# Kernel optimization log

Hardware: AMD Instinct MI355X
Metric: run time of the kernel (lower is better)

## Reference

```python
import jax, jax.numpy as jnp
import numpy as np

B = 32
HIST, C, H, W = 10, 11, 15, 20
D, NH, NL = 256, 4, 4
HD = D // NH
OUT, ADIM = 256, 20
L = HIST * H * W + 1  # 3001 tokens incl. cls
VIS = HIST * C * H * W  # 33000


def layernorm(x, g, b, eps=1e-5):
    m = jnp.mean(x, axis=-1, keepdims=True)
    v = jnp.mean((x - m) ** 2, axis=-1, keepdims=True)
    return (x - m) * jax.lax.rsqrt(v + eps) * g + b


def rope_1d(x):
    # x: [B, NH, L, HD]
    l, hd = x.shape[2], x.shape[3]
    t = jnp.arange(l, dtype=x.dtype)
    freqs = 10000.0 ** (-jnp.arange(0, hd, 2, dtype=x.dtype) / hd)
    emb = t[:, None] * freqs[None, :]            # [L, HD/2]
    emb = jnp.concatenate([emb, emb], axis=-1)   # [L, HD]
    cos = jnp.cos(emb)[None, None]
    sin = jnp.sin(emb)[None, None]
    x1, x2 = x[..., : hd // 2], x[..., hd // 2 :]
    rot = jnp.concatenate([-x2, x1], axis=-1)
    return x * cos + rot * sin


def lightning_attn(x, qw, kw, vw, ow, gq, bq, gk, bk):
    b, l, _ = x.shape
    q = layernorm(x @ qw, gq, bq)
    k = layernorm(x @ kw, gk, bk)
    v = x @ vw
    split = lambda a: a.reshape(b, l, NH, HD).transpose(0, 2, 1, 3)  # [B,NH,L,HD]
    q, k, v = split(q), split(k), split(v)
    q = jax.nn.silu(rope_1d(q))
    k = jax.nn.silu(rope_1d(k))
    kv = jnp.einsum('bhld,bhle->bhde', k, v)            # O(L) kv accumulation
    out = jnp.einsum('bhld,bhde->bhle', q, kv)
    out = out / jnp.sqrt(jnp.asarray(HD, x.dtype))
    out = out.transpose(0, 2, 1, 3).reshape(b, l, D)
    return out @ ow


def forward(obs_stack, proj_w, proj_b, cls_token, qw, kw, vw, ow, gq, bq, gk, bk,
            n1g, n1b, n2g, n2b, w1, b1, w2, b2, fng, fnb, out_w, out_b):
    b = obs_stack.shape[0]
    obs_feat = obs_stack[:, :VIS]
    action_feat = obs_stack[:, VIS:]
    vision = obs_feat.reshape(b, HIST, C, H, W).transpose(0, 1, 3, 4, 2)  # [B,T,H,W,C]
    x = vision @ proj_w + proj_b                                          # [B,T,H,W,D]
    x = x.reshape(b, -1, D)
    cls = jnp.broadcast_to(cls_token, (b, 1, D))
    x = jnp.concatenate([cls, x], axis=1)                                 # [B,L,D]
    for i in range(NL):
        h = lightning_attn(layernorm(x, n1g[i], n1b[i]), qw[i], kw[i], vw[i], ow[i],
                           gq[i], bq[i], gk[i], bk[i])
        x = x + h
        y = layernorm(x, n2g[i], n2b[i])
        y = jax.nn.gelu(y @ w1[i] + b1[i], approximate=False) @ w2[i] + b2[i]
        x = x + y
    x = layernorm(x, fng, fnb)
    cls_out = x[:, 0, :]
    final = jnp.concatenate([cls_out, action_feat], axis=1)
    return final @ out_w + out_b


def setup_inputs() -> dict:
    key = jax.random.key(0)
    ks = jax.random.split(key, 16)
    s = 0.02
    n = lambda k, shp: jax.random.normal(k, shp, dtype=jnp.float32) * s
    inp = {
        'obs_stack': jax.random.normal(ks[0], (B, VIS + ADIM), dtype=jnp.float32),
        'proj_w': n(ks[1], (C, D)),
        'proj_b': jnp.zeros((D,), jnp.float32),
        'cls_token': jax.random.normal(ks[2], (1, 1, D), dtype=jnp.float32),
        'qw': n(ks[3], (NL, D, D)),
        'kw': n(ks[4], (NL, D, D)),
        'vw': n(ks[5], (NL, D, D)),
        'ow': n(ks[6], (NL, D, D)),
        'gq': jnp.ones((NL, D), jnp.float32),
        'bq': jnp.zeros((NL, D), jnp.float32),
        'gk': jnp.ones((NL, D), jnp.float32),
        'bk': jnp.zeros((NL, D), jnp.float32),
        'n1g': jnp.ones((NL, D), jnp.float32),
        'n1b': jnp.zeros((NL, D), jnp.float32),
        'n2g': jnp.ones((NL, D), jnp.float32),
        'n2b': jnp.zeros((NL, D), jnp.float32),
        'w1': n(ks[7], (NL, D, 4 * D)),
        'b1': jnp.zeros((NL, 4 * D), jnp.float32),
        'w2': n(ks[8], (NL, 4 * D, D)),
        'b2': jnp.zeros((NL, D), jnp.float32),
        'fng': jnp.ones((D,), jnp.float32),
        'fnb': jnp.zeros((D,), jnp.float32),
        'out_w': n(ks[9], (D + ADIM, OUT)),
        'out_b': jnp.zeros((OUT,), jnp.float32),
    }
    return inp


def reference(obs_stack, proj_w, proj_b, cls_token, qw, kw, vw, ow, gq, bq, gk, bk,
              n1g, n1b, n2g, n2b, w1, b1, w2, b2, fng, fnb, out_w, out_b):
    return forward(obs_stack, proj_w, proj_b, cls_token, qw, kw, vw, ow, gq, bq, gk, bk,
                   n1g, n1b, n2g, n2b, w1, b1, w2, b2, fng, fnb, out_w, out_b)
```

## Files before the change

### kernel.cpp

```cpp
#include <hip/hip_runtime.h>
#include <math.h>

typedef unsigned short u16;
typedef __attribute__((ext_vector_type(8))) short short8;
typedef __attribute__((ext_vector_type(4))) short short4v;
typedef __attribute__((ext_vector_type(4))) float f32x4;

constexpr int B_    = 32;
constexpr int HIST_ = 10, C_ = 11, H_ = 15, W_ = 20;
constexpr int D_    = 256, NH_ = 4, NL_ = 4, HD_ = 64;
constexpr int OUT_  = 256, ADIM_ = 20;
constexpr int L_    = HIST_*H_*W_ + 1;
constexpr int VIS_  = HIST_*C_*H_*W_;
constexpr int NTOK  = B_*L_;
constexpr int OBSROW = VIS_ + ADIM_;
constexpr int PADR  = 128;

__device__ __forceinline__ float bf2f(u16 u) {
    return __uint_as_float(((unsigned)u) << 16);
}
__device__ __forceinline__ u16 f2bf(float f) {
    unsigned u = __float_as_uint(f);
    u = u + 0x7FFFu + ((u >> 16) & 1u);
    return (u16)(u >> 16);
}
__device__ __forceinline__ f32x4 mfma16(short8 a, short8 b, f32x4 c) {
    return __builtin_amdgcn_mfma_f32_16x16x32_bf16(a, b, c, 0, 0, 0);
}
__device__ __forceinline__ void gload16(const u16* gsrc, u16* ldsdst) {
    __builtin_amdgcn_global_load_lds(
        (const __attribute__((address_space(1))) unsigned int*)gsrc,
        (__attribute__((address_space(3))) unsigned int*)ldsdst,
        16, 0, 0);
}
__device__ __forceinline__ float gelu_fast(float v) {
    float t2 = 1.5957691216f*(v + 0.044715f*v*v*v);
    return v / (1.f + __expf(-t2));
}

__global__ void zero_kernel(float* __restrict__ p, int n) {
    int i = blockIdx.x*256 + threadIdx.x;
    if (i < n) p[i] = 0.f;
}

__global__ void wcvt_kernel(const float* __restrict__ src, u16* __restrict__ dst,
                            int Nn, int Kk, int dstLS, int dstOff) {
    int idx = blockIdx.x*256 + threadIdx.x;
    int tot = NL_*Nn*Kk;
    if (idx >= tot) return;
    int l = idx / (Nn*Kk);
    int rem = idx % (Nn*Kk);
    int n = rem / Kk, k = rem % Kk;
    dst[(size_t)l*dstLS + (size_t)(dstOff+n)*Kk + k] = f2bf(src[(size_t)l*Kk*Nn + (size_t)k*Nn + n]);
}

__global__ void rope_table_kernel(float* __restrict__ tab) {
    int idx = blockIdx.x*256 + threadIdx.x;
    if (idx >= L_*32) return;
    int t = idx >> 5, i = idx & 31;
    float freq = powf(10000.f, -2.f*(float)i/(float)HD_);
    float ang = (float)t * freq;
    tab[idx*2]   = cosf(ang);
    tab[idx*2+1] = sinf(ang);
}

__global__ __launch_bounds__(256) void proj_kernel(const float* __restrict__ obs,
        const float* __restrict__ pw, const float* __restrict__ pb,
        const float* __restrict__ cls, float* __restrict__ x) {
    int wave = threadIdx.x >> 6, lane = threadIdx.x & 63;
    int n = blockIdx.x*4 + wave;
    if (n >= NTOK) return;
    int b = n / L_, l = n % L_;
    float4 acc;
    if (l == 0) {
        acc = ((const float4*)cls)[lane];
    } else {
        int t = l - 1;
        int hist = t / (H_*W_);
        int rem  = t % (H_*W_);
        float vv = 0.f;
        if (lane < C_) vv = obs[(size_t)b*OBSROW + hist*(C_*H_*W_) + lane*(H_*W_) + rem];
        acc = ((const float4*)pb)[lane];
        #pragma unroll
        for (int c = 0; c < C_; ++c) {
            float vc = __shfl(vv, c);
            float4 w4 = ((const float4*)(pw + c*D_))[lane];
            acc.x += vc*w4.x; acc.y += vc*w4.y; acc.z += vc*w4.z; acc.w += vc*w4.w;
        }
    }
    ((float4*)(x + (size_t)n*D_))[lane] = acc;
}

__global__ __launch_bounds__(256) void ln_f2b_kernel(const float* __restrict__ in,
        const float* __restrict__ g, const float* __restrict__ bt,
        u16* __restrict__ out, int ntok) {
    int wave = threadIdx.x >> 6, lane = threadIdx.x & 63;
    int n = blockIdx.x*4 + wave;
    if (n >= ntok) return;
    float4 v = ((const float4*)(in + (size_t)n*D_))[lane];
    float s  = v.x + v.y + v.z + v.w;
    float sq = v.x*v.x + v.y*v.y + v.z*v.z + v.w*v.w;
    #pragma unroll
    for (int off = 32; off; off >>= 1) { s += __shfl_xor(s, off); sq += __shfl_xor(sq, off); }
    float mean = s * (1.f/D_);
    float var  = sq * (1.f/D_) - mean*mean;
    float r = rsqrtf(var + 1e-5f);
    float4 gg = ((const float4*)g)[lane];
    float4 bb = ((const float4*)bt)[lane];
    short4v o;
    o.x = (short)f2bf((v.x-mean)*r*gg.x + bb.x);
    o.y = (short)f2bf((v.y-mean)*r*gg.y + bb.y);
    o.z = (short)f2bf((v.z-mean)*r*gg.z + bb.z);
    o.w = (short)f2bf((v.w-mean)*r*gg.w + bb.w);
    *(short4v*)(out + (size_t)n*D_ + lane*4) = o;
}

__global__ __launch_bounds__(256) void lnres_kernel(float* __restrict__ x,
        u16* __restrict__ dx, const float* __restrict__ g, const float* __restrict__ bt,
        int ntok) {
    int wave = threadIdx.x >> 6, lane = threadIdx.x & 63;
    int n = blockIdx.x*4 + wave;
    if (n >= ntok) return;
    float4 v = ((const float4*)(x + (size_t)n*D_))[lane];
    short4v d = *(const short4v*)(dx + (size_t)n*D_ + lane*4);
    v.x += bf2f((u16)d.x); v.y += bf2f((u16)d.y);
    v.z += bf2f((u16)d.z); v.w += bf2f((u16)d.w);
    ((float4*)(x + (size_t)n*D_))[lane] = v;
    float s  = v.x + v.y + v.z + v.w;
    float sq = v.x*v.x + v.y*v.y + v.z*v.z + v.w*v.w;
    #pragma unroll
    for (int off = 32; off; off >>= 1) { s += __shfl_xor(s, off); sq += __shfl_xor(sq, off); }
    float mean = s * (1.f/D_);
    float var  = sq * (1.f/D_) - mean*mean;
    float r = rsqrtf(var + 1e-5f);
    float4 gg = ((const float4*)g)[lane];
    float4 bb = ((const float4*)bt)[lane];
    short4v o;
    o.x = (short)f2bf((v.x-mean)*r*gg.x + bb.x);
    o.y = (short)f2bf((v.y-mean)*r*gg.y + bb.y);
    o.z = (short)f2bf((v.z-mean)*r*gg.z + bb.z);
    o.w = (short)f2bf((v.w-mean)*r*gg.w + bb.w);
    *(short4v*)(dx + (size_t)n*D_ + lane*4) = o;
}

__global__ __launch_bounds__(256) void lnrope_kernel(u16* __restrict__ qk,
        const float* __restrict__ gq, const float* __restrict__ bq,
        const float* __restrict__ gk, const float* __restrict__ bk,
        const float* __restrict__ tab, int ntok, int ld) {
    u16* q = qk + blockIdx.y*256;
    const float* g  = blockIdx.y ? gk : gq;
    const float* bt = blockIdx.y ? bk : bq;
    int wave = threadIdx.x >> 6, lane = threadIdx.x & 63;
    int n = blockIdx.x*4 + wave;
    if (n >= ntok) return;
    int l = n % L_;
    short4v raw = *(const short4v*)(q + (size_t)n*ld + lane*4);
    float v0 = bf2f((u16)raw.x), v1 = bf2f((u16)raw.y), v2 = bf2f((u16)raw.z), v3 = bf2f((u16)raw.w);
    float s  = v0+v1+v2+v3;
    float sq = v0*v0+v1*v1+v2*v2+v3*v3;
    #pragma unroll
    for (int off = 32; off; off >>= 1) { s += __shfl_xor(s, off); sq += __shfl_xor(sq, off); }
    float mean = s * (1.f/D_);
    float var  = sq * (1.f/D_) - mean*mean;
    float r = rsqrtf(var + 1e-5f);
    float4 gg = ((const float4*)g)[lane];
    float4 bb = ((const float4*)bt)[lane];
    float o0 = (v0-mean)*r*gg.x + bb.x;
    float o1 = (v1-mean)*r*gg.y + bb.y;
    float o2 = (v2-mean)*r*gg.z + bb.z;
    float o3 = (v3-mean)*r*gg.w + bb.w;
    float p0 = __shfl_xor(o0, 8), p1 = __shfl_xor(o1, 8);
    float p2 = __shfl_xor(o2, 8), p3 = __shfl_xor(o3, 8);
    bool first = (lane & 15) < 8;
    const float4* tp = (const float4*)(tab + ((size_t)l*32 + (lane&7)*4)*2);
    float4 t01 = tp[0], t23 = tp[1];
    float r0 = first ? o0*t01.x - p0*t01.y : o0*t01.x + p0*t01.y;
    float r1 = first ? o1*t01.z - p1*t01.w : o1*t01.z + p1*t01.w;
    float r2 = first ? o2*t23.x - p2*t23.y : o2*t23.x + p2*t23.y;
    float r3 = first ? o3*t23.z - p3*t23.w : o3*t23.z + p3*t23.w;
    r0 = r0 / (1.f + expf(-r0));
    r1 = r1 / (1.f + expf(-r1));
    r2 = r2 / (1.f + expf(-r2));
    r3 = r3 / (1.f + expf(-r3));
    short4v o;
    o.x = (short)f2bf(r0); o.y = (short)f2bf(r1);
    o.z = (short)f2bf(r2); o.w = (short)f2bf(r3);
    *(short4v*)(q + (size_t)n*ld + lane*4) = o;
}

template<int EPI, bool PB>
__global__ __launch_bounds__(256) void gemm_bf16(const u16* __restrict__ A, int lda,
        const u16* __restrict__ Wt, const float* __restrict__ bias,
        u16* __restrict__ Cb, float* __restrict__ Xres, int M, int N, int K, int ldc) {
    __shared__ u16 As[2*128*32];
    __shared__ u16 Bs[2*128*32];
    const int gx = gridDim.x;
    int n = blockIdx.y * gx + blockIdx.x;
    const int nwg = gx * gridDim.y;
    if ((nwg & 7) == 0) n = (n & 7) * (nwg >> 3) + (n >> 3);
    const int bx = n % gx, by = n / gx;
    const int row0 = by*128, col0 = bx*128;

    size_t zrow = 0;
    if (PB) {
        int z = blockIdx.z;
        A  += (size_t)z * M * lda;
        Wt += (size_t)z * N * K;
        zrow = (size_t)z * M;
    }

    const int tid = threadIdx.x;
    const int wid = tid >> 6, lane = tid & 63;
    const int wr = wid >> 1, wc = wid & 1;

    f32x4 acc[4][4];
    #pragma unroll
    for (int i = 0; i < 4; ++i)
        #pragma unroll
        for (int j = 0; j < 4; ++j) {
            f32x4 z; z.x = 0.f; z.y = 0.f; z.z = 0.f; z.w = 0.f;
            acc[i][j] = z;
        }

    const int r0s = wid*32 + (lane>>2);
    const int r1s = r0s + 16;
    const int s0 = ((lane&3) - (r0s>>1)) & 3;
    const int s1 = ((lane&3) - (r1s>>1)) & 3;
    const u16* a0p = A  + (size_t)(row0 + r0s)*lda + s0*8;
    const u16* a1p = A  + (size_t)(row0 + r1s)*lda + s1*8;
    const u16* b0p = Wt + (size_t)(col0 + r0s)*K + s0*8;
    const u16* b1p = Wt + (size_t)(col0 + r1s)*K + s1*8;
    u16* lA0 = As + (wid*2+0)*512;
    u16* lA1 = As + (wid*2+1)*512;
    u16* lB0 = Bs + (wid*2+0)*512;
    u16* lB1 = Bs + (wid*2+1)*512;

    const int kg = lane >> 4, li = lane & 15;
    int aoff[4], boff[4];
    #pragma unroll
    for (int mi = 0; mi < 4; ++mi) {
        int row = wr*64 + mi*16 + li;
        aoff[mi] = row*32 + ((kg + (row>>1)) & 3)*8;
    }
    #pragma unroll
    for (int ni = 0; ni < 4; ++ni) {
        int row = wc*64 + ni*16 + li;
        boff[ni] = row*32 + ((kg + (row>>1)) & 3)*8;
    }

    auto stage = [&](int k0) {
        #pragma unroll
        for (int t = 0; t < 2; ++t) {
            const int ko = k0 + t*32;
            const int lo = t*4096;
            gload16(a0p + ko, lA0 + lo); gload16(a1p + ko, lA1 + lo);
            gload16(b0p + ko, lB0 + lo); gload16(b1p + ko, lB1 + lo);
        }
    };

    stage(0);
    const int nk2 = K >> 6;
    for (int ks = 0; ks < nk2; ++ks) {
        __syncthreads();
        short8 af[2][4], bfr[2][4];
        #pragma unroll
        for (int t = 0; t < 2; ++t) {
            #pragma unroll
            for (int mi = 0; mi < 4; ++mi) af[t][mi] = *(const short8*)(As + t*4096 + aoff[mi]);
            #pragma unroll
            for (int ni = 0; ni < 4; ++ni) bfr[t][ni] = *(const short8*)(Bs + t*4096 + boff[ni]);
        }
        __syncthreads();
        if (ks + 1 < nk2) stage((ks + 1) << 6);
        #pragma unroll
        for (int t = 0; t < 2; ++t)
            #pragma unroll
            for (int mi = 0; mi < 4; ++mi)
                #pragma unroll
                for (int ni = 0; ni < 4; ++ni)
                    acc[mi][ni] = mfma16(af[t][mi], bfr[t][ni], acc[mi][ni]);
    }

    #pragma unroll
    for (int mi = 0; mi < 4; ++mi) {
        int rbase = row0 + wr*64 + mi*16 + kg*4;
        #pragma unroll
        for (int ni = 0; ni < 4; ++ni) {
            int col = col0 + wc*64 + ni*16 + li;
            #pragma unroll
            for (int r = 0; r < 4; ++r) {
                int row = rbase + r;
                if (row >= M) continue;
                float v = acc[mi][ni][r];
                if (EPI == 1 || EPI == 4) v += bias[col];
                if (EPI == 1) v = gelu_fast(v);
                Cb[(zrow + row)*(size_t)ldc + col] = f2bf(v);
            }
        }
    }
}

template<int EPI, bool PB>
__global__ __launch_bounds__(512) void gemm_wide(const u16* __restrict__ A, int lda,
        const u16* __restrict__ Wt, const float* __restrict__ bias,
        u16* __restrict__ Cb, int M, int N, int K, int ldc) {
    __shared__ u16 As[2*4096];
    __shared__ u16 Bs[2*8192];
    const int gx = gridDim.x;
    int n = blockIdx.y * gx + blockIdx.x;
    const int nwg = gx * gridDim.y;
    if ((nwg & 7) == 0) n = (n & 7) * (nwg >> 3) + (n >> 3);
    const int bx = n % gx, by = n / gx;
    const int row0 = by*128, col0 = bx*256;

    size_t zrow = 0;
    if (PB) {
        int z = blockIdx.z;
        A  += (size_t)z * M * lda;
        Wt += (size_t)z * N * K;
        zrow = (size_t)z * M;
    }

    const int tid = threadIdx.x;
    const int wid = tid >> 6, lane = tid & 63;
    const int kg = lane >> 4, li = lane & 15;

    f32x4 acc[16];
    #pragma unroll
    for (int i = 0; i < 16; ++i) { f32x4 z; z.x=0.f; z.y=0.f; z.z=0.f; z.w=0.f; acc[i]=z; }

    const int ra = wid*16 + (lane>>2);
    const int sa = ((lane&3) - (ra>>1)) & 3;
    const u16* agp = A + (size_t)(row0 + ra)*lda + sa*8;
    const int lAo = wid*512;
    const int rb0 = (wid*2+0)*16 + (lane>>2);
    const int rb1 = (wid*2+1)*16 + (lane>>2);
    const int sb0 = ((lane&3) - (rb0>>1)) & 3;
    const int sb1 = ((lane&3) - (rb1>>1)) & 3;
    const u16* bgp0 = Wt + (size_t)(col0 + rb0)*K + sb0*8;
    const u16* bgp1 = Wt + (size_t)(col0 + rb1)*K + sb1*8;
    const int lB0o = (wid*2+0)*512;
    const int lB1o = (wid*2+1)*512;

    const int arow = wid*16 + li;
    const int aoff = arow*32 + ((kg + (arow>>1)) & 3)*8;
    int boff[16];
    #pragma unroll
    for (int ni = 0; ni < 16; ++ni) {
        int row = ni*16 + li;
        boff[ni] = row*32 + ((kg + (row>>1)) & 3)*8;
    }

    auto stage = [&](int k0) {
        #pragma unroll
        for (int t = 0; t < 2; ++t) {
            const int ko = k0 + t*32;
            gload16(agp  + ko, As + t*4096 + lAo);
            gload16(bgp0 + ko, Bs + t*8192 + lB0o);
            gload16(bgp1 + ko, Bs + t*8192 + lB1o);
        }
    };

    stage(0);
    const int nk2 = K >> 6;
    for (int ks = 0; ks < nk2; ++ks) {
        __syncthreads();
        short8 af0 = *(const short8*)(As + aoff);
        short8 b0[8], b1[8];
        #pragma unroll
        for (int ni = 0; ni < 8; ++ni) b0[ni] = *(const short8*)(Bs + boff[ni]);
        #pragma unroll
        for (int ni = 0; ni < 8; ++ni) acc[ni] = mfma16(af0, b0[ni], acc[ni]);
        #pragma unroll
        for (int ni = 0; ni < 8; ++ni) b1[ni] = *(const short8*)(Bs + boff[8+ni]);
        #pragma unroll
        for (int ni = 0; ni < 8; ++ni) acc[8+ni] = mfma16(af0, b1[ni], acc[8+ni]);
        short8 af1 = *(const short8*)(As + 4096 + aoff);
        #pragma unroll
        for (int ni = 0; ni < 8; ++ni) b0[ni] = *(const short8*)(Bs + 8192 + boff[ni]);
        #pragma unroll
        for (int ni = 0; ni < 8; ++ni) b1[ni] = *(const short8*)(Bs + 8192 + boff[8+ni]);
        __syncthreads();
        if (ks + 1 < nk2) stage((ks + 1) << 6);
        #pragma unroll
        for (int ni = 0; ni < 8; ++ni) acc[ni]   = mfma16(af1, b0[ni], acc[ni]);
        #pragma unroll
        for (int ni = 0; ni < 8; ++ni) acc[8+ni] = mfma16(af1, b1[ni], acc[8+ni]);
    }

    #pragma unroll
    for (int r = 0; r < 4; ++r) {
        const int row = row0 + wid*16 + kg*4 + r;
        if (row >= M) continue;
        #pragma unroll
        for (int ni = 0; ni < 16; ++ni) {
            int col = col0 + ni*16 + li;
            float v = acc[ni][r];
            if (EPI == 1) { v += bias[col]; v = gelu_fast(v); }
            Cb[(zrow + row)*(size_t)ldc + col] = f2bf(v);
        }
    }
}

constexpr int KV_LSPLIT = 4;
constexpr int KV_PART   = 768;
__global__ __launch_bounds__(256) void kv_mfma_kernel(const u16* __restrict__ Kt,
        const u16* __restrict__ Vt, float* __restrict__ kvf, int ld) {
    __shared__ u16 kT[64][34];
    __shared__ u16 vT[64][34];
    const int bh = blockIdx.x;
    const int b = bh >> 2, h = bh & 3;
    const int tid = threadIdx.x;
    const int wid = tid >> 6, lane = tid & 63;
    const int kg = lane >> 4, li = lane & 15;
    const int wm = (wid >> 1)*32, wn = (wid & 1)*32;
    const int sl = tid >> 3;
    const int sd = (tid & 7) * 8;
    const u16* kbase = Kt + ((size_t)b*L_)*ld + h*HD_ + sd;
    const u16* vbase = Vt + ((size_t)b*L_)*ld + h*HD_ + sd;

    f32x4 acc[2][2];
    #pragma unroll
    for (int i = 0; i < 2; ++i)
        #pragma unroll
        for (int j = 0; j < 2; ++j) {
            f32x4 z; z.x=0.f; z.y=0.f; z.z=0.f; z.w=0.f; acc[i][j] = z;
        }

    const int l0p = blockIdx.y * KV_PART;
    for (int t = 0; t < KV_PART/32; ++t) {
        int gl = l0p + t*32 + sl;
        short8 kk = {0,0,0,0,0,0,0,0}, vv = {0,0,0,0,0,0,0,0};
        if (gl < L_) {
            kk = *(const short8*)(kbase + (size_t)gl*ld);
            vv = *(const short8*)(vbase + (size_t)gl*ld);
        }
        __syncthreads();
        #pragma unroll
        for (int j = 0; j < 8; ++j) {
            kT[sd+j][sl] = (u16)kk[j];
            vT[sd+j][sl] = (u16)vv[j];
        }
        __syncthreads();
        short8 a0, a1, b0, b1;
        {
            uint* d0 = (uint*)&a0; const uint* p0 = (const uint*)&kT[wm + li][kg*8];
            uint* d1 = (uint*)&a1; const uint* p1 = (const uint*)&kT[wm + 16 + li][kg*8];
            uint* d2 = (uint*)&b0; const uint* p2 = (const uint*)&vT[wn + li][kg*8];
            uint* d3 = (uint*)&b1; const uint* p3 = (const uint*)&vT[wn + 16 + li][kg*8];
            #pragma unroll
            for (int j = 0; j < 4; ++j) { d0[j]=p0[j]; d1[j]=p1[j]; d2[j]=p2[j]; d3[j]=p3[j]; }
        }
        acc[0][0] = mfma16(a0, b0, acc[0][0]);
        acc[0][1] = mfma16(a0, b1, acc[0][1]);
        acc[1][0] = mfma16(a1, b0, acc[1][0]);
        acc[1][1] = mfma16(a1, b1, acc[1][1]);
    }
    float* base = kvf + (size_t)bh*4096;
    #pragma unroll
    for (int mi = 0; mi < 2; ++mi)
        #pragma unroll
        for (int ni = 0; ni < 2; ++ni)
            #pragma unroll
            for (int r = 0; r < 4; ++r)
                atomicAdd(base + (wm + mi*16 + kg*4 + r)*64 + wn + ni*16 + li,
                          acc[mi][ni][r]);
}

__global__ __launch_bounds__(256) void m2_kernel(const float* __restrict__ kvf,
        const float* __restrict__ ow, u16* __restrict__ m2t) {
    __shared__ float kvs[64][64];
    const int bh = blockIdx.x;
    const int b = bh >> 2, h = bh & 3;
    const int tid = threadIdx.x;
    #pragma unroll
    for (int p = 0; p < 16; ++p)
        ((float*)kvs)[p*256 + tid] = kvf[(size_t)bh*4096 + p*256 + tid];
    __syncthreads();
    float acc[64];
    #pragma unroll
    for (int d = 0; d < 64; ++d) acc[d] = 0.f;
    for (int e = 0; e < 64; ++e) {
        float w = ow[(size_t)(h*64 + e)*256 + tid];
        #pragma unroll
        for (int d = 0; d < 64; ++d) acc[d] += kvs[d][e] * w;
    }
    u16* dst = m2t + ((size_t)b*256 + tid)*256 + h*64;
    #pragma unroll
    for (int d = 0; d < 64; ++d) dst[d] = f2bf(acc[d]*0.125f);
}

__global__ __launch_bounds__(256) void tail_kernel(const u16* __restrict__ Xn,
        const u16* __restrict__ qwT,
        const float* __restrict__ gqv, const float* __restrict__ bqv,
        const u16* __restrict__ m2t, float* __restrict__ x,
        const float* __restrict__ g2, const float* __restrict__ bt2,
        const u16* __restrict__ w1T, const float* __restrict__ b1v,
        const u16* __restrict__ w2T, const float* __restrict__ b2v) {
    __shared__ float xn0[256];
    __shared__ float qrow[256];
    __shared__ float y[256];
    __shared__ float h[1024];
    __shared__ float red[8];
    const int bl = blockIdx.x;
    const int tid = threadIdx.x;
    const int wave = tid >> 6, lane = tid & 63;
    const size_t row = (size_t)bl * L_;
    xn0[tid] = bf2f(Xn[row*256 + tid]);
    __syncthreads();
    {
        const u16* qwrow = qwT + (size_t)tid*256;
        float qa = 0.f;
        for (int k = 0; k < 256; k += 8) {
            short8 w = *(const short8*)(qwrow + k);
            qa += xn0[k+0]*bf2f((u16)w[0]) + xn0[k+1]*bf2f((u16)w[1])
                + xn0[k+2]*bf2f((u16)w[2]) + xn0[k+3]*bf2f((u16)w[3])
                + xn0[k+4]*bf2f((u16)w[4]) + xn0[k+5]*bf2f((u16)w[5])
                + xn0[k+6]*bf2f((u16)w[6]) + xn0[k+7]*bf2f((u16)w[7]);
        }
        float s = qa, sq = qa*qa;
        #pragma unroll
        for (int off = 32; off; off >>= 1) { s += __shfl_xor(s, off); sq += __shfl_xor(sq, off); }
        if (lane == 0) { red[wave] = s; red[4+wave] = sq; }
        __syncthreads();
        s  = red[0]+red[1]+red[2]+red[3];
        sq = red[4]+red[5]+red[6]+red[7];
        float mean = s*(1.f/256.f), var = sq*(1.f/256.f) - mean*mean;
        float rstd = rsqrtf(var + 1e-5f);
        float qn = (qa - mean)*rstd*gqv[tid] + bqv[tid];
        qrow[tid] = qn / (1.f + __expf(-qn));
    }
    __syncthreads();
    const u16* mrow = m2t + ((size_t)bl*256 + tid)*256;
    float acc = 0.f;
    for (int d = 0; d < 256; d += 8) {
        short8 w = *(const short8*)(mrow + d);
        acc += qrow[d+0]*bf2f((u16)w[0]) + qrow[d+1]*bf2f((u16)w[1])
             + qrow[d+2]*bf2f((u16)w[2]) + qrow[d+3]*bf2f((u16)w[3])
             + qrow[d+4]*bf2f((u16)w[4]) + qrow[d+5]*bf2f((u16)w[5])
             + qrow[d+6]*bf2f((u16)w[6]) + qrow[d+7]*bf2f((u16)w[7]);
    }
    float v = x[row*256 + tid] + acc;
    float s = v, sq = v*v;
    #pragma unroll
    for (int off = 32; off; off >>= 1) { s += __shfl_xor(s, off); sq += __shfl_xor(sq, off); }
    if (lane == 0) { red[wave] = s; red[4+wave] = sq; }
    __syncthreads();
    s  = red[0]+red[1]+red[2]+red[3];
    sq = red[4]+red[5]+red[6]+red[7];
    float mean = s*(1.f/256.f), var = sq*(1.f/256.f) - mean*mean;
    float rstd = rsqrtf(var + 1e-5f);
    y[tid] = (v - mean)*rstd*g2[tid] + bt2[tid];
    __syncthreads();
    #pragma unroll
    for (int jj = 0; jj < 4; ++jj) {
        int j = tid*4 + jj;
        const u16* wrow = w1T + (size_t)j*256;
        float a = b1v[j];
        for (int k = 0; k < 256; k += 8) {
            short8 w = *(const short8*)(wrow + k);
            a += y[k+0]*bf2f((u16)w[0]) + y[k+1]*bf2f((u16)w[1])
               + y[k+2]*bf2f((u16)w[2]) + y[k+3]*bf2f((u16)w[3])
               + y[k+4]*bf2f((u16)w[4]) + y[k+5]*bf2f((u16)w[5])
               + y[k+6]*bf2f((u16)w[6]) + y[k+7]*bf2f((u16)w[7]);
        }
        h[j] = gelu_fast(a);
    }
    __syncthreads();
    const u16* w2row = w2T + (size_t)tid*1024;
    float a2 = b2v[tid];
    for (int k = 0; k < 1024; k += 8) {
        short8 w = *(const short8*)(w2row + k);
        a2 += h[k+0]*bf2f((u16)w[0]) + h[k+1]*bf2f((u16)w[1])
            + h[k+2]*bf2f((u16)w[2]) + h[k+3]*bf2f((u16)w[3])
            + h[k+4]*bf2f((u16)w[4]) + h[k+5]*bf2f((u16)w[5])
            + h[k+6]*bf2f((u16)w[6]) + h[k+7]*bf2f((u16)w[7]);
    }
    x[row*256 + tid] = v + a2;
}

__global__ void head_kernel(const float* __restrict__ x, const float* __restrict__ obs,
                            const float* __restrict__ fng, const float* __restrict__ fnb,
                            const float* __restrict__ ow, const float* __restrict__ ob,
                            float* __restrict__ out) {
    __shared__ float row[D_ + ADIM_];
    __shared__ float red[8];
    int b = blockIdx.x, tid = threadIdx.x;
    float v = x[((size_t)b*L_)*D_ + tid];
    float s = v, sq = v*v;
    #pragma unroll
    for (int off = 32; off; off >>= 1) { s += __shfl_xor(s, off); sq += __shfl_xor(sq, off); }
    int wave = tid >> 6, lane = tid & 63;
    if (lane == 0) { red[wave] = s; red[4+wave] = sq; }
    __syncthreads();
    s  = red[0]+red[1]+red[2]+red[3];
    sq = red[4]+red[5]+red[6]+red[7];
    float mean = s*(1.f/D_), var = sq*(1.f/D_) - mean*mean;
    float r = rsqrtf(var + 1e-5f);
    row[tid] = (v-mean)*r*fng[tid] + fnb[tid];
    if (tid < ADIM_) row[D_+tid] = obs[(size_t)b*OBSROW + VIS_ + tid];
    __syncthreads();
    float acc = ob[tid];
    for (int j = 0; j < D_+ADIM_; ++j) acc += row[j]*ow[j*OUT_ + tid];
    out[(size_t)b*OUT_ + tid] = acc;
}

extern "C" void kernel_launch(void* const* d_in, const int* in_sizes, int n_in,
                              void* d_out, int out_size, void* d_ws, size_t ws_size,
                              hipStream_t stream) {
    const float* obs   = (const float*)d_in[0];
    const float* pw    = (const float*)d_in[1];
    const float* pb    = (const float*)d_in[2];
    const float* cls   = (const float*)d_in[3];
    const float* qw    = (const float*)d_in[4];
    const float* kw    = (const float*)d_in[5];
    const float* vw    = (const float*)d_in[6];
    const float* oww   = (const float*)d_in[7];
    const float* gq    = (const float*)d_in[8];
    const float* bq    = (const float*)d_in[9];
    const float* gk    = (const float*)d_in[10];
    const float* bk    = (const float*)d_in[11];
    const float* n1g   = (const float*)d_in[12];
    const float* n1b   = (const float*)d_in[13];
    const float* n2g   = (const float*)d_in[14];
    const float* n2b   = (const float*)d_in[15];
    const float* w1    = (const float*)d_in[16];
    const float* b1    = (const float*)d_in[17];
    const float* w2    = (const float*)d_in[18];
    const float* b2    = (const float*)d_in[19];
    const float* fng   = (const float*)d_in[20];
    const float* fnb   = (const float*)d_in[21];
    const float* outw  = (const float*)d_in[22];
    const float* outb  = (const float*)d_in[23];

    float* x = (float*)d_ws;
    u16* qkvT = (u16*)(x + (size_t)NTOK*D_);
    u16* w1T  = qkvT + (size_t)NL_*768*256;
    u16* w2T  = w1T  + (size_t)NL_*262144;
    float* tab = (float*)(w2T + (size_t)NL_*262144);
    u16* bufs = (u16*)(tab + (size_t)L_*32*2);

    size_t fixedB = (size_t)((char*)bufs - (char*)d_ws);
    auto needed = [&](int nb) -> size_t {
        size_t t = (size_t)nb * L_;
        return fixedB + (t*256 + (size_t)PADR*256)*2 + (t*1024 + (size_t)PADR*1024)*2
               + (size_t)nb*65536*2 + (size_t)nb*NH_*4096*4;
    };
    int nbc = 32;
    while (nbc > 1 && needed(nbc) > ws_size) nbc >>= 1;
    const int nch = B_ / nbc;
    const int RCn = nbc * L_;

    u16* Xn   = bufs;
    u16* QKVc = Xn + (size_t)RCn*256 + (size_t)PADR*256;
    u16* Hc   = QKVc;
    u16* M2T  = QKVc + (size_t)RCn*1024 + (size_t)PADR*1024;
    float* kvf = (float*)(M2T + (size_t)nbc*65536);

    wcvt_kernel<<<(NL_*65536 + 255)/256, 256, 0, stream>>>(qw,  qkvT, 256, 256, 768*256, 0);
    wcvt_kernel<<<(NL_*65536 + 255)/256, 256, 0, stream>>>(kw,  qkvT, 256, 256, 768*256, 256);
    wcvt_kernel<<<(NL_*65536 + 255)/256, 256, 0, stream>>>(vw,  qkvT, 256, 256, 768*256, 512);
    wcvt_kernel<<<(NL_*262144 + 255)/256, 256, 0, stream>>>(w1, w1T, 1024, 256, 262144, 0);
    wcvt_kernel<<<(NL_*262144 + 255)/256, 256, 0, stream>>>(w2, w2T, 256, 1024, 262144, 0);
    rope_table_kernel<<<(L_*32 + 255)/256, 256, 0, stream>>>(tab);
    proj_kernel<<<(NTOK + 3)/4, 256, 0, stream>>>(obs, pw, pb, cls, x);

    const int gy  = (RCn + 127)/128;
    const int lnb = (RCn + 3)/4;
    const int nbh = nbc*NH_;

    for (int c = 0; c < nch; ++c) {
        float* xc = x + (size_t)c*RCn*D_;
        ln_f2b_kernel<<<lnb, 256, 0, stream>>>(xc, n1g, n1b, Xn, RCn);

        for (int layer = 0; layer < NL_; ++layer) {
            const u16* qkvT_l = qkvT + (size_t)layer*768*256;
            const u16* w1T_l  = w1T  + (size_t)layer*262144;
            const u16* w2T_l  = w2T  + (size_t)layer*262144;
            const float* ow_l = oww + (size_t)layer*65536;
            const float* b1_l = b1 + (size_t)layer*1024;
            const float* b2_l = b2 + (size_t)layer*D_;

            if (layer < NL_-1) {
                gemm_wide<0,false><<<dim3(3, gy), 512, 0, stream>>>(Xn, 256, qkvT_l, nullptr, QKVc, RCn, 768, 256, 768);
                lnrope_kernel<<<dim3(lnb, 2), 256, 0, stream>>>(QKVc, gq + layer*D_, bq + layer*D_,
                                                                gk + layer*D_, bk + layer*D_, tab, RCn, 768);
            } else {
                gemm_wide<0,false><<<dim3(2, gy), 512, 0, stream>>>(Xn, 256, qkvT_l + 65536, nullptr, QKVc + 256, RCn, 512, 256, 768);
                lnrope_kernel<<<dim3(lnb, 1), 256, 0, stream>>>(QKVc + 256, gk + layer*D_, bk + layer*D_,
                                                                gk + layer*D_, bk + layer*D_, tab, RCn, 768);
            }
            zero_kernel<<<(nbh*4096 + 255)/256, 256, 0, stream>>>(kvf, nbh*4096);
            kv_mfma_kernel<<<dim3(nbh, KV_LSPLIT), 256, 0, stream>>>(QKVc + 256, QKVc + 512, kvf, 768);
            m2_kernel<<<nbh, 256, 0, stream>>>(kvf, ow_l, M2T);

            if (layer < NL_-1) {
                gemm_bf16<0,true><<<dim3(2, 24, nbc), 256, 0, stream>>>(QKVc, 768, M2T, nullptr, Xn, nullptr, L_, 256, 256, 256);
                lnres_kernel<<<lnb, 256, 0, stream>>>(xc, Xn, n2g + layer*D_, n2b + layer*D_, RCn);
                gemm_wide<1,false><<<dim3(4, gy), 512, 0, stream>>>(Xn, 256, w1T_l, b1_l, Hc, RCn, 1024, 256, 1024);
                gemm_bf16<4,false><<<dim3(2, gy), 256, 0, stream>>>(Hc, 1024, w2T_l, b2_l, Xn, nullptr, RCn, 256, 1024, 256);
                lnres_kernel<<<lnb, 256, 0, stream>>>(xc, Xn, n1g + (layer+1)*D_, n1b + (layer+1)*D_, RCn);
            } else {
                tail_kernel<<<nbc, 256, 0, stream>>>(Xn, qkvT_l, gq + layer*D_, bq + layer*D_,
                                                     M2T, xc, n2g + layer*D_, n2b + layer*D_,
                                                     w1T_l, b1_l, w2T_l, b2_l);
            }
        }
    }

    head_kernel<<<B_, 256, 0, stream>>>(x, obs, fng, fnb, outw, outb, (float*)d_out);
}
```

Before: 2.245 ms.

## Store residual stream in bf16 and hoist kv accumulator zeroing

```diff
diff --git a/kernel.cpp b/kernel.cpp
--- a/kernel.cpp
+++ b/kernel.cpp
@@ -66,7 +66,7 @@
 
 __global__ __launch_bounds__(256) void proj_kernel(const float* __restrict__ obs,
         const float* __restrict__ pw, const float* __restrict__ pb,
-        const float* __restrict__ cls, float* __restrict__ x) {
+        const float* __restrict__ cls, u16* __restrict__ x) {
     int wave = threadIdx.x >> 6, lane = threadIdx.x & 63;
     int n = blockIdx.x*4 + wave;
     if (n >= NTOK) return;
@@ -88,18 +88,22 @@
             acc.x += vc*w4.x; acc.y += vc*w4.y; acc.z += vc*w4.z; acc.w += vc*w4.w;
         }
     }
-    ((float4*)(x + (size_t)n*D_))[lane] = acc;
-}
-
-__global__ __launch_bounds__(256) void ln_f2b_kernel(const float* __restrict__ in,
+    short4v o;
+    o.x = (short)f2bf(acc.x); o.y = (short)f2bf(acc.y);
+    o.z = (short)f2bf(acc.z); o.w = (short)f2bf(acc.w);
+    *(short4v*)(x + (size_t)n*D_ + lane*4) = o;
+}
+
+__global__ __launch_bounds__(256) void ln_f2b_kernel(const u16* __restrict__ in,
         const float* __restrict__ g, const float* __restrict__ bt,
         u16* __restrict__ out, int ntok) {
     int wave = threadIdx.x >> 6, lane = threadIdx.x & 63;
     int n = blockIdx.x*4 + wave;
     if (n >= ntok) return;
-    float4 v = ((const float4*)(in + (size_t)n*D_))[lane];
-    float s  = v.x + v.y + v.z + v.w;
-    float sq = v.x*v.x + v.y*v.y + v.z*v.z + v.w*v.w;
+    short4v raw = *(const short4v*)(in + (size_t)n*D_ + lane*4);
+    float v0 = bf2f((u16)raw.x), v1 = bf2f((u16)raw.y), v2 = bf2f((u16)raw.z), v3 = bf2f((u16)raw.w);
+    float s  = v0+v1+v2+v3;
+    float sq = v0*v0+v1*v1+v2*v2+v3*v3;
     #pragma unroll
     for (int off = 32; off; off >>= 1) { s += __shfl_xor(s, off); sq += __shfl_xor(sq, off); }
     float mean = s * (1.f/D_);
@@ -108,26 +112,31 @@
     float4 gg = ((const float4*)g)[lane];
     float4 bb = ((const float4*)bt)[lane];
     short4v o;
-    o.x = (short)f2bf((v.x-mean)*r*gg.x + bb.x);
-    o.y = (short)f2bf((v.y-mean)*r*gg.y + bb.y);
-    o.z = (short)f2bf((v.z-mean)*r*gg.z + bb.z);
-    o.w = (short)f2bf((v.w-mean)*r*gg.w + bb.w);
+    o.x = (short)f2bf((v0-mean)*r*gg.x + bb.x);
+    o.y = (short)f2bf((v1-mean)*r*gg.y + bb.y);
+    o.z = (short)f2bf((v2-mean)*r*gg.z + bb.z);
+    o.w = (short)f2bf((v3-mean)*r*gg.w + bb.w);
     *(short4v*)(out + (size_t)n*D_ + lane*4) = o;
 }
 
-__global__ __launch_bounds__(256) void lnres_kernel(float* __restrict__ x,
+__global__ __launch_bounds__(256) void lnres_kernel(u16* __restrict__ x,
         u16* __restrict__ dx, const float* __restrict__ g, const float* __restrict__ bt,
         int ntok) {
     int wave = threadIdx.x >> 6, lane = threadIdx.x & 63;
     int n = blockIdx.x*4 + wave;
     if (n >= ntok) return;
-    float4 v = ((const float4*)(x + (size_t)n*D_))[lane];
-    short4v d = *(const short4v*)(dx + (size_t)n*D_ + lane*4);
-    v.x += bf2f((u16)d.x); v.y += bf2f((u16)d.y);
-    v.z += bf2f((u16)d.z); v.w += bf2f((u16)d.w);
-    ((float4*)(x + (size_t)n*D_))[lane] = v;
-    float s  = v.x + v.y + v.z + v.w;
-    float sq = v.x*v.x + v.y*v.y + v.z*v.z + v.w*v.w;
+    short4v xv = *(const short4v*)(x + (size_t)n*D_ + lane*4);
+    short4v d  = *(const short4v*)(dx + (size_t)n*D_ + lane*4);
+    float v0 = bf2f((u16)xv.x) + bf2f((u16)d.x);
+    float v1 = bf2f((u16)xv.y) + bf2f((u16)d.y);
+    float v2 = bf2f((u16)xv.z) + bf2f((u16)d.z);
+    float v3 = bf2f((u16)xv.w) + bf2f((u16)d.w);
+    short4v xo;
+    xo.x = (short)f2bf(v0); xo.y = (short)f2bf(v1);
+    xo.z = (short)f2bf(v2); xo.w = (short)f2bf(v3);
+    *(short4v*)(x + (size_t)n*D_ + lane*4) = xo;
+    float s  = v0+v1+v2+v3;
+    float sq = v0*v0+v1*v1+v2*v2+v3*v3;
     #pragma unroll
     for (int off = 32; off; off >>= 1) { s += __shfl_xor(s, off); sq += __shfl_xor(sq, off); }
     float mean = s * (1.f/D_);
@@ -136,10 +145,10 @@
     float4 gg = ((const float4*)g)[lane];
     float4 bb = ((const float4*)bt)[lane];
     short4v o;
-    o.x = (short)f2bf((v.x-mean)*r*gg.x + bb.x);
-    o.y = (short)f2bf((v.y-mean)*r*gg.y + bb.y);
-    o.z = (short)f2bf((v.z-mean)*r*gg.z + bb.z);
-    o.w = (short)f2bf((v.w-mean)*r*gg.w + bb.w);
+    o.x = (short)f2bf((v0-mean)*r*gg.x + bb.x);
+    o.y = (short)f2bf((v1-mean)*r*gg.y + bb.y);
+    o.z = (short)f2bf((v2-mean)*r*gg.z + bb.z);
+    o.w = (short)f2bf((v3-mean)*r*gg.w + bb.w);
     *(short4v*)(dx + (size_t)n*D_ + lane*4) = o;
 }
 
@@ -493,7 +502,7 @@
 __global__ __launch_bounds__(256) void tail_kernel(const u16* __restrict__ Xn,
         const u16* __restrict__ qwT,
         const float* __restrict__ gqv, const float* __restrict__ bqv,
-        const u16* __restrict__ m2t, float* __restrict__ x,
+        const u16* __restrict__ m2t, u16* __restrict__ x,
         const float* __restrict__ g2, const float* __restrict__ bt2,
         const u16* __restrict__ w1T, const float* __restrict__ b1v,
         const u16* __restrict__ w2T, const float* __restrict__ b2v) {
@@ -540,7 +549,7 @@
              + qrow[d+4]*bf2f((u16)w[4]) + qrow[d+5]*bf2f((u16)w[5])
              + qrow[d+6]*bf2f((u16)w[6]) + qrow[d+7]*bf2f((u16)w[7]);
     }
-    float v = x[row*256 + tid] + acc;
+    float v = bf2f(x[row*256 + tid]) + acc;
     float s = v, sq = v*v;
     #pragma unroll
     for (int off = 32; off; off >>= 1) { s += __shfl_xor(s, off); sq += __shfl_xor(sq, off); }
@@ -576,17 +585,17 @@
             + h[k+4]*bf2f((u16)w[4]) + h[k+5]*bf2f((u16)w[5])
             + h[k+6]*bf2f((u16)w[6]) + h[k+7]*bf2f((u16)w[7]);
     }
-    x[row*256 + tid] = v + a2;
-}
-
-__global__ void head_kernel(const float* __restrict__ x, const float* __restrict__ obs,
+    x[row*256 + tid] = f2bf(v + a2);
+}
+
+__global__ void head_kernel(const u16* __restrict__ x, const float* __restrict__ obs,
                             const float* __restrict__ fng, const float* __restrict__ fnb,
                             const float* __restrict__ ow, const float* __restrict__ ob,
                             float* __restrict__ out) {
     __shared__ float row[D_ + ADIM_];
     __shared__ float red[8];
     int b = blockIdx.x, tid = threadIdx.x;
-    float v = x[((size_t)b*L_)*D_ + tid];
+    float v = bf2f(x[((size_t)b*L_)*D_ + tid]);
     float s = v, sq = v*v;
     #pragma unroll
     for (int off = 32; off; off >>= 1) { s += __shfl_xor(s, off); sq += __shfl_xor(sq, off); }
@@ -633,18 +642,19 @@
     const float* outw  = (const float*)d_in[22];
     const float* outb  = (const float*)d_in[23];
 
-    float* x = (float*)d_ws;
-    u16* qkvT = (u16*)(x + (size_t)NTOK*D_);
+    u16* x    = (u16*)d_ws;
+    u16* qkvT = x + (size_t)NTOK*D_;
     u16* w1T  = qkvT + (size_t)NL_*768*256;
     u16* w2T  = w1T  + (size_t)NL_*262144;
     float* tab = (float*)(w2T + (size_t)NL_*262144);
-    u16* bufs = (u16*)(tab + (size_t)L_*32*2);
+    float* kvf_all = tab + (size_t)L_*32*2;
+    u16* bufs = (u16*)(kvf_all + (size_t)NL_*B_*NH_*4096);
 
     size_t fixedB = (size_t)((char*)bufs - (char*)d_ws);
     auto needed = [&](int nb) -> size_t {
         size_t t = (size_t)nb * L_;
         return fixedB + (t*256 + (size_t)PADR*256)*2 + (t*1024 + (size_t)PADR*1024)*2
-               + (size_t)nb*65536*2 + (size_t)nb*NH_*4096*4;
+               + (size_t)nb*65536*2;
     };
     int nbc = 32;
     while (nbc > 1 && needed(nbc) > ws_size) nbc >>= 1;
@@ -655,7 +665,6 @@
     u16* QKVc = Xn + (size_t)RCn*256 + (size_t)PADR*256;
     u16* Hc   = QKVc;
     u16* M2T  = QKVc + (size_t)RCn*1024 + (size_t)PADR*1024;
-    float* kvf = (float*)(M2T + (size_t)nbc*65536);
 
     wcvt_kernel<<<(NL_*65536 + 255)/256, 256, 0, stream>>>(qw,  qkvT, 256, 256, 768*256, 0);
     wcvt_kernel<<<(NL_*65536 + 255)/256, 256, 0, stream>>>(kw,  qkvT, 256, 256, 768*256, 256);
@@ -663,6 +672,7 @@
     wcvt_kernel<<<(NL_*262144 + 255)/256, 256, 0, stream>>>(w1, w1T, 1024, 256, 262144, 0);
     wcvt_kernel<<<(NL_*262144 + 255)/256, 256, 0, stream>>>(w2, w2T, 256, 1024, 262144, 0);
     rope_table_kernel<<<(L_*32 + 255)/256, 256, 0, stream>>>(tab);
+    zero_kernel<<<(NL_*B_*NH_*4096 + 255)/256, 256, 0, stream>>>(kvf_all, NL_*B_*NH_*4096);
     proj_kernel<<<(NTOK + 3)/4, 256, 0, stream>>>(obs, pw, pb, cls, x);
 
     const int gy  = (RCn + 127)/128;
@@ -670,7 +680,7 @@
     const int nbh = nbc*NH_;
 
     for (int c = 0; c < nch; ++c) {
-        float* xc = x + (size_t)c*RCn*D_;
+        u16* xc = x + (size_t)c*RCn*D_;
         ln_f2b_kernel<<<lnb, 256, 0, stream>>>(xc, n1g, n1b, Xn, RCn);
 
         for (int layer = 0; layer < NL_; ++layer) {
@@ -680,6 +690,7 @@
             const float* ow_l = oww + (size_t)layer*65536;
             const float* b1_l = b1 + (size_t)layer*1024;
             const float* b2_l = b2 + (size_t)layer*D_;
+            float* kvf = kvf_all + ((size_t)(c*NL_ + layer))*nbh*4096;
 
             if (layer < NL_-1) {
                 gemm_wide<0,false><<<dim3(3, gy), 512, 0, stream>>>(Xn, 256, qkvT_l, nullptr, QKVc, RCn, 768, 256, 768);
@@ -690,7 +701,6 @@
                 lnrope_kernel<<<dim3(lnb, 1), 256, 0, stream>>>(QKVc + 256, gk + layer*D_, bk + layer*D_,
                                                                 gk + layer*D_, bk + layer*D_, tab, RCn, 768);
             }
-            zero_kernel<<<(nbh*4096 + 255)/256, 256, 0, stream>>>(kvf, nbh*4096);
             kv_mfma_kernel<<<dim3(nbh, KV_LSPLIT), 256, 0, stream>>>(QKVc + 256, QKVc + 512, kvf, 768);
             m2_kernel<<<nbh, 256, 0, stream>>>(kvf, ow_l, M2T);
 
```

Measured after the change: 2.144 ms. 4.5% less time.
